# Kernel optimization log

Hardware: AMD Instinct MI355X
Metric: run time of the kernel (lower is better)

The kernel has to match this reference:

```python
import jax, jax.numpy as jnp
import numpy as np

N_HEAD = 16
ROPE_BASE = 10000.0


def rotate_half(x):
    d = x.shape[-1] // 2
    return jnp.concatenate((-x[..., d:], x[..., :d]), axis=-1)


def rope_cos_sin(T, head_dim, dtype):
    inv_freq = 1.0 / (ROPE_BASE ** (jnp.arange(0, head_dim, 2, dtype=jnp.float32) / head_dim))
    t = jnp.arange(T, dtype=jnp.float32)
    freqs = jnp.einsum('i,j->ij', t, inv_freq)  # [T, head_dim/2]
    emb = jnp.concatenate((freqs, freqs), axis=-1)  # [T, head_dim]
    return jnp.cos(emb).astype(dtype), jnp.sin(emb).astype(dtype)


def setup_inputs() -> dict:
    key = jax.random.key(0)
    k1, k2, k3 = jax.random.split(key, 3)
    B, T, C = 4, 2048, 2048
    x = jax.random.normal(k1, (B, T, C), dtype=jnp.float32)
    w_attn = jax.random.normal(k2, (3 * C, C), dtype=jnp.float32) * (1.0 / np.sqrt(C))
    w_proj = jax.random.normal(k3, (C, C), dtype=jnp.float32) * (1.0 / np.sqrt(C))
    return {"x": x, "w_attn": w_attn, "w_proj": w_proj}


def reference(x, w_attn, w_proj):
    B, T, C = x.shape
    H = N_HEAD
    D = C // H
    qkv = jnp.einsum('btc,fc->btf', x, w_attn)  # [B, T, 3C]
    q, k, v = jnp.split(qkv, 3, axis=-1)
    # [B, H, T, D]
    q = q.reshape(B, T, H, D).transpose(0, 2, 1, 3)
    k = k.reshape(B, T, H, D).transpose(0, 2, 1, 3)
    v = v.reshape(B, T, H, D).transpose(0, 2, 1, 3)
    cos, sin = rope_cos_sin(T, D, x.dtype)  # [T, D]
    cos = cos[None, None, :, :]
    sin = sin[None, None, :, :]
    q = q * cos + rotate_half(q) * sin
    k = k * cos + rotate_half(k) * sin
    # bidirectional SDPA
    scale = 1.0 / jnp.sqrt(jnp.asarray(D, dtype=x.dtype))
    att = jnp.einsum('bhtd,bhsd->bhts', q, k) * scale
    att = jax.nn.softmax(att, axis=-1)
    y = jnp.einsum('bhts,bhsd->bhtd', att, v)
    y = y.transpose(0, 2, 1, 3).reshape(B, T, C)
    return jnp.einsum('btc,oc->bto', y, w_proj)
```

## Files before the change

kernel.cpp:

```cpp
#include <hip/hip_runtime.h>

#define DEVINL __device__ __forceinline__

typedef unsigned short u16;
typedef __attribute__((ext_vector_type(8))) __bf16 bf16x8;
typedef __attribute__((ext_vector_type(4))) float f32x4;
typedef __attribute__((ext_vector_type(16))) float f32x16;

struct alignas(8) u16x4 { u16 x, y, z, w; };

#define MFMA16(a, b, c) __builtin_amdgcn_mfma_f32_16x16x32_bf16(a, b, c, 0, 0, 0)
#define MFMA32(a, b, c) __builtin_amdgcn_mfma_f32_32x32x16_bf16(a, b, c, 0, 0, 0)

DEVINL u16 f2bf(float f) {
  unsigned u = __builtin_bit_cast(unsigned, f);
  u += 0x7fffu + ((u >> 16) & 1u);
  return (u16)(u >> 16);
}

DEVINL unsigned cvtpk_bf16(float lo, float hi) {
  unsigned r;
  asm("v_cvt_pk_bf16_f32 %0, %1, %2" : "=v"(r) : "v"(lo), "v"(hi));
  return r;
}

DEVINL void plane_swap(unsigned& a, unsigned& b) {
  asm("v_permlane32_swap_b32 %0, %1" : "+v"(a), "+v"(b));
}

DEVINL void gload_lds16(const u16* g, u16* l) {
  __builtin_amdgcn_global_load_lds((const __attribute__((address_space(1))) void*)g,
                                   (__attribute__((address_space(3))) void*)l,
                                   16, 0, 0);
}

DEVINL bf16x8 frag64(const u16* lds, int row, int cg) {
  int c = cg ^ (row & 7);
  return *(const bf16x8*)(lds + row * 64 + c * 8);
}
DEVINL bf16x8 frag128(const u16* lds, int row, int cg) {
  int c = cg ^ (row & 7);
  return *(const bf16x8*)(lds + row * 128 + c * 8);
}

DEVINL void stage_k512(const u16* g, u16* lds, int wave, int lane) {
#pragma unroll
  for (int t = 0; t < 2; ++t) {
    int r = t * 32 + wave * 4 + (lane >> 4);
    int cg = (lane & 15) ^ (r & 7);
    gload_lds16(g + (size_t)r * 128 + cg * 8, lds + (t * 32 + wave * 4) * 128);
  }
}
DEVINL void stage_v512(const u16* g, int ldg, u16* lds, int wave, int lane) {
#pragma unroll
  for (int t = 0; t < 2; ++t) {
    int r = t * 64 + wave * 8 + (lane >> 3);
    int cg = (lane & 7) ^ (r & 7);
    gload_lds16(g + (size_t)r * ldg + cg * 8, lds + (t * 64 + wave * 8) * 64);
  }
}

DEVINL int perm32(int row) { return (row & 3) ^ ((row >> 2) & 3); }

DEVINL void stage32(const u16* g, int ldg, u16* lds, int q, int wave, int lane) {
  int row = q * 128 + wave * 16 + (lane >> 2);
  int cg = (lane & 3) ^ perm32(row);
  gload_lds16(g + (size_t)row * ldg + cg * 8, lds + (q * 128 + wave * 16) * 32);
}

DEVINL bf16x8 frag32(const u16* lds, int row, int lc) {
  int c = lc ^ perm32(row);
  return *(const bf16x8*)(lds + row * 32 + c * 8);
}

__global__ void __launch_bounds__(256) k_cast(const float* __restrict__ src,
                                              u16* __restrict__ dst, int n4) {
  int i = blockIdx.x * blockDim.x + threadIdx.x;
  int stride = gridDim.x * blockDim.x;
  for (; i < n4; i += stride) {
    float4 f = ((const float4*)src)[i];
    u16x4 u;
    u.x = f2bf(f.x); u.y = f2bf(f.y); u.z = f2bf(f.z); u.w = f2bf(f.w);
    ((u16x4*)dst)[i] = u;
  }
}

DEVINL void gemm_loop256(const u16* Ag, const u16* Bg, int K, u16* smem,
                         f32x4 acc[8][4], int wave, int lane) {
  const int wm = wave >> 2, wn = wave & 3;
  const int lr = lane & 15, lc = lane >> 4;

#pragma unroll
  for (int t = 0; t < 3; ++t) {
    u16* At = smem + t * 8192;
    u16* Bt = smem + 32768 + t * 8192;
    stage32(Ag + t * 32, K, At, 0, wave, lane);
    stage32(Ag + t * 32, K, At, 1, wave, lane);
    stage32(Bg + t * 32, K, Bt, 0, wave, lane);
    stage32(Bg + t * 32, K, Bt, 1, wave, lane);
  }
  asm volatile("s_waitcnt vmcnt(8)" ::: "memory");
  asm volatile("s_barrier" ::: "memory");

  bf16x8 bfr[4], aA[4], aB[4];
#pragma unroll
  for (int nf = 0; nf < 4; ++nf)
    bfr[nf] = frag32(smem + 32768, nf * 64 + wn * 16 + lr, lc);
#pragma unroll
  for (int mf = 0; mf < 4; ++mf)
    aA[mf] = frag32(smem, wm * 128 + mf * 16 + lr, lc);

  const int nsteps = K / 32;
  for (int s = 0; s < nsteps; ++s) {
    const int slot = s & 3;
    const u16* Ac = smem + slot * 8192;
    const bool do_stage = (s + 3 < nsteps);
    u16* An = smem + ((s + 3) & 3) * 8192;
    u16* Bn = smem + 32768 + ((s + 3) & 3) * 8192;
    const u16* Agn = Ag + (size_t)(s + 3) * 32;
    const u16* Bgn = Bg + (size_t)(s + 3) * 32;

    __builtin_amdgcn_s_setprio(1);
#pragma unroll
    for (int mf = 0; mf < 4; ++mf)
#pragma unroll
      for (int nf = 0; nf < 4; ++nf)
        acc[mf][nf] = MFMA16(aA[mf], bfr[nf], acc[mf][nf]);
    __builtin_amdgcn_s_setprio(0);
#pragma unroll
    for (int mf = 0; mf < 4; ++mf)
      aB[mf] = frag32(Ac, wm * 128 + (mf + 4) * 16 + lr, lc);
    if (do_stage) {
      stage32(Agn, K, An, 0, wave, lane);
      stage32(Agn, K, An, 1, wave, lane);
    }
    if (s + 3 < nsteps) {
      asm volatile("s_waitcnt vmcnt(6)" ::: "memory");
    } else if (s + 2 < nsteps) {
      asm volatile("s_waitcnt vmcnt(4)" ::: "memory");
    } else if (s + 1 < nsteps) {
      asm volatile("s_waitcnt vmcnt(0)" ::: "memory");
    }
    asm volatile("s_barrier" ::: "memory");

    __builtin_amdgcn_s_setprio(1);
#pragma unroll
    for (int mf = 0; mf < 4; ++mf)
#pragma unroll
      for (int nf = 0; nf < 4; ++nf)
        acc[mf + 4][nf] = MFMA16(aB[mf], bfr[nf], acc[mf + 4][nf]);
    __builtin_amdgcn_s_setprio(0);
    if (s + 1 < nsteps) {
      const int slot1 = (s + 1) & 3;
      const u16* An1 = smem + slot1 * 8192;
      const u16* Bn1 = smem + 32768 + slot1 * 8192;
#pragma unroll
      for (int nf = 0; nf < 4; ++nf)
        bfr[nf] = frag32(Bn1, nf * 64 + wn * 16 + lr, lc);
#pragma unroll
      for (int mf = 0; mf < 4; ++mf)
        aA[mf] = frag32(An1, wm * 128 + mf * 16 + lr, lc);
    }
    if (do_stage) {
      stage32(Bgn, K, Bn, 0, wave, lane);
      stage32(Bgn, K, Bn, 1, wave, lane);
    }
    asm volatile("s_barrier" ::: "memory");
  }
}

__global__ void __launch_bounds__(512, 2) k_gemm_qkv(const u16* __restrict__ xb,
                                                     const u16* __restrict__ wab,
                                                     u16* __restrict__ qb,
                                                     u16* __restrict__ kb,
                                                     u16* __restrict__ vtb) {
  extern __shared__ u16 smem[];
  int bid = blockIdx.x;
  const int xcd = bid & 7, local = bid >> 3;
  const int tm = (xcd & 3) * 8 + (local & 7);
  const int tn = (xcd >> 2) * 12 + (local >> 3);
  const int wave = threadIdx.x >> 6, lane = threadIdx.x & 63;
  const int wm = wave >> 2, wn = wave & 3;
  const int lr = lane & 15, lc = lane >> 4;

  f32x4 acc[8][4];
#pragma unroll
  for (int i = 0; i < 8; ++i)
#pragma unroll
    for (int n = 0; n < 4; ++n) acc[i][n] = f32x4{0.f, 0.f, 0.f, 0.f};

  gemm_loop256(xb + (size_t)tm * 256 * 2048, wab + (size_t)tn * 256 * 2048, 2048,
               smem, acc, wave, lane);

  const int sel = tn >> 3;
  const int hh = (tn & 7) * 2;
  const int m0 = tm * 256 + wm * 128;
  const int b = (tm * 256) >> 11;

  if (sel < 2) {
    u16* dst = sel ? kb : qb;
    const float qs = sel ? 1.0f : 0.12751745f;
    const int d = wn * 16 + lr;
    const float invf = __expf(-0.14391156631f * (float)d);
#pragma unroll
    for (int mf = 0; mf < 8; ++mf) {
#pragma unroll
      for (int j = 0; j < 4; ++j) {
        int t = (m0 + mf * 16 + lc * 4 + j) & 2047;
        float ang = (float)t * invf;
        float s, c;
        __sincosf(ang, &s, &c);
#pragma unroll
        for (int hp = 0; hp < 2; ++hp) {
          float lo = acc[mf][2 * hp][j];
          float hi = acc[mf][2 * hp + 1][j];
          size_t rowp = ((size_t)(b * 16 + hh + hp) * 2048 + t) * 128;
          dst[rowp + d] = f2bf((lo * c - hi * s) * qs);
          dst[rowp + d + 64] = f2bf((hi * c + lo * s) * qs);
        }
      }
    }
  } else {
#pragma unroll
    for (int mf = 0; mf < 8; ++mf) {
      int t0 = (m0 + mf * 16 + lc * 4) & 2047;
#pragma unroll
      for (int nf = 0; nf < 4; ++nf) {
        int d = wn * 16 + lr + (nf & 1) * 64;
        int h = hh + (nf >> 1);
        u16x4 pk;
        pk.x = f2bf(acc[mf][nf][0]);
        pk.y = f2bf(acc[mf][nf][1]);
        pk.z = f2bf(acc[mf][nf][2]);
        pk.w = f2bf(acc[mf][nf][3]);
        *(u16x4*)(vtb + ((size_t)(b * 16 + h) * 128 + d) * 2048 + t0) = pk;
      }
    }
  }
}

__global__ void __launch_bounds__(512, 2) k_gemm_proj(const u16* __restrict__ yb,
                                                      const u16* __restrict__ wpb,
                                                      float* __restrict__ out) {
  extern __shared__ u16 smem[];
  int bid = blockIdx.x;
  int sw = (bid & 7) * 32 + (bid >> 3);
  const int tm = sw >> 3, tn = sw & 7;
  const int wave = threadIdx.x >> 6, lane = threadIdx.x & 63;
  const int wm = wave >> 2, wn = wave & 3;
  const int lr = lane & 15, lc = lane >> 4;

  f32x4 acc[8][4];
#pragma unroll
  for (int i = 0; i < 8; ++i)
#pragma unroll
    for (int n = 0; n < 4; ++n) acc[i][n] = f32x4{0.f, 0.f, 0.f, 0.f};

  gemm_loop256(yb + (size_t)tm * 256 * 2048, wpb + (size_t)tn * 256 * 2048, 2048,
               smem, acc, wave, lane);

  const int m0 = tm * 256 + wm * 128;
#pragma unroll
  for (int mf = 0; mf < 8; ++mf) {
#pragma unroll
    for (int j = 0; j < 4; ++j) {
      int gr = m0 + mf * 16 + lc * 4 + j;
      float* op = out + (size_t)gr * 2048 + tn * 256 + wn * 16 + lr;
#pragma unroll
      for (int nf = 0; nf < 4; ++nf) op[nf * 64] = acc[mf][nf][j];
    }
  }
}

__global__ void __launch_bounds__(512) k_attn(const u16* __restrict__ qg,
                                              const u16* __restrict__ kg,
                                              const u16* __restrict__ vtg,
                                              u16* __restrict__ yg) {
  __shared__ u16 Ks[2][64 * 128];
  __shared__ u16 Vs[2][128 * 64];
  int bid = blockIdx.x;
  int sw = (bid & 7) * 64 + (bid >> 3);
  const int qt = sw & 7, bh = sw >> 3;
  const int wave = threadIdx.x >> 6, lane = threadIdx.x & 63;
  const int hi = lane >> 5, ln = lane & 31;

  const u16* qbh = qg + (size_t)bh * (2048 * 128);
  const u16* kbh = kg + (size_t)bh * (2048 * 128);
  const u16* vbh = vtg + (size_t)bh * (128 * 2048);
  const int qrow0 = qt * 256 + wave * 32;

  bf16x8 qf[8];
#pragma unroll
  for (int kc = 0; kc < 8; ++kc)
    qf[kc] = *(const bf16x8*)(qbh + (size_t)(qrow0 + ln) * 128 + kc * 16 + hi * 8);

  f32x16 yacc[4];
#pragma unroll
  for (int nd = 0; nd < 4; ++nd)
#pragma unroll
    for (int r = 0; r < 16; ++r) yacc[nd][r] = 0.f;
  float m = -1e30f, l = 0.f;

  stage_k512(kbh, Ks[0], wave, lane);
  stage_v512(vbh, 2048, Vs[0], wave, lane);
  __syncthreads();

  int buf = 0;
  for (int kv0 = 0; kv0 < 2048; kv0 += 64) {
    if (kv0 + 64 < 2048) {
      stage_k512(kbh + (size_t)(kv0 + 64) * 128, Ks[buf ^ 1], wave, lane);
      stage_v512(vbh + kv0 + 64, 2048, Vs[buf ^ 1], wave, lane);
    }
    const u16* Kb = Ks[buf];
    const u16* Vb = Vs[buf];

    f32x16 st[2];
#pragma unroll
    for (int h2 = 0; h2 < 2; ++h2)
#pragma unroll
      for (int r = 0; r < 16; ++r) st[h2][r] = 0.f;
    __builtin_amdgcn_s_setprio(1);
#pragma unroll
    for (int kc = 0; kc < 8; ++kc) {
      bf16x8 a0 = frag128(Kb, ln, kc * 2 + hi);
      bf16x8 a1 = frag128(Kb, 32 + ln, kc * 2 + hi);
      st[0] = MFMA32(a0, qf[kc], st[0]);
      st[1] = MFMA32(a1, qf[kc], st[1]);
    }
    __builtin_amdgcn_s_setprio(0);

    float t8[8];
#pragma unroll
    for (int i = 0; i < 8; ++i)
      t8[i] = fmaxf(fmaxf(st[0][i], st[0][i + 8]), fmaxf(st[1][i], st[1][i + 8]));
    float pmax = fmaxf(fmaxf(fmaxf(t8[0], t8[4]), fmaxf(t8[1], t8[5])),
                       fmaxf(fmaxf(t8[2], t8[6]), fmaxf(t8[3], t8[7])));
    pmax = fmaxf(pmax, __shfl_xor(pmax, 32));

    if (__any(pmax - m > 11.5415603f)) {
      float mn = fmaxf(m, pmax);
      float al = __builtin_amdgcn_exp2f(m - mn);
      m = mn;
      l *= al;
#pragma unroll
      for (int nd = 0; nd < 4; ++nd)
#pragma unroll
        for (int r = 0; r < 16; ++r) yacc[nd][r] *= al;
    }

    float sa0 = 0.f, sa1 = 0.f, sa2 = 0.f, sa3 = 0.f;
#pragma unroll
    for (int h2 = 0; h2 < 2; ++h2) {
#pragma unroll
      for (int r = 0; r < 16; ++r) {
        float e = __builtin_amdgcn_exp2f(st[h2][r] - m);
        st[h2][r] = e;
        if ((r & 3) == 0) sa0 += e;
        else if ((r & 3) == 1) sa1 += e;
        else if ((r & 3) == 2) sa2 += e;
        else sa3 += e;
      }
    }
    float ssum = (sa0 + sa1) + (sa2 + sa3);
    ssum += __shfl_xor(ssum, 32);
    l += ssum;

    unsigned wa[2][4], wb[2][4];
#pragma unroll
    for (int h2 = 0; h2 < 2; ++h2)
#pragma unroll
      for (int q8 = 0; q8 < 4; ++q8) {
        wa[h2][q8] = cvtpk_bf16(st[h2][q8 * 4 + 0], st[h2][q8 * 4 + 1]);
        wb[h2][q8] = cvtpk_bf16(st[h2][q8 * 4 + 2], st[h2][q8 * 4 + 3]);
      }

    __builtin_amdgcn_s_setprio(1);
#pragma unroll
    for (int ks = 0; ks < 4; ++ks) {
      const int h2 = ks >> 1, k1 = ks & 1;
      unsigned w0 = wa[h2][2 * k1], w2 = wa[h2][2 * k1 + 1];
      plane_swap(w0, w2);
      unsigned w1 = wb[h2][2 * k1], w3 = wb[h2][2 * k1 + 1];
      plane_swap(w1, w3);
      union { unsigned u[4]; bf16x8 v; } pa;
      pa.u[0] = w0; pa.u[1] = w1; pa.u[2] = w2; pa.u[3] = w3;
#pragma unroll
      for (int nd = 0; nd < 4; ++nd) {
        bf16x8 bv = frag64(Vb, nd * 32 + ln, 2 * ks + hi);
        yacc[nd] = MFMA32(pa.v, bv, yacc[nd]);
      }
    }
    __builtin_amdgcn_s_setprio(0);

    __syncthreads();
    buf ^= 1;
  }

  const int b = bh >> 4, h = bh & 15;
  float inv = 1.f / l;
#pragma unroll
  for (int r = 0; r < 16; ++r) {
    int crow = (r & 3) + 8 * (r >> 2) + 4 * hi;
    float li = __shfl(inv, crow);
    int t = qrow0 + crow;
    size_t rp = ((size_t)b * 2048 + t) * 2048 + h * 128;
#pragma unroll
    for (int nd = 0; nd < 4; ++nd)
      yg[rp + nd * 32 + ln] = f2bf(yacc[nd][r] * li);
  }
}

extern "C" void kernel_launch(void* const* d_in, const int* in_sizes, int n_in,
                              void* d_out, int out_size, void* d_ws, size_t ws_size,
                              hipStream_t stream) {
  const float* x = (const float*)d_in[0];
  const float* wa = (const float*)d_in[1];
  const float* wp = (const float*)d_in[2];
  float* out = (float*)d_out;

  u16* xb = (u16*)d_ws;
  u16* wab = xb + 16777216;
  u16* wpb = wab + 12582912;
  u16* qb = wpb + 4194304;
  u16* kb = qb + 16777216;
  u16* vtb = kb + 16777216;
  u16* yb = vtb + 16777216;

  hipFuncSetAttribute((const void*)k_gemm_qkv,
                      hipFuncAttributeMaxDynamicSharedMemorySize, 131072);
  hipFuncSetAttribute((const void*)k_gemm_proj,
                      hipFuncAttributeMaxDynamicSharedMemorySize, 131072);

  k_cast<<<dim3(2048), dim3(256), 0, stream>>>(x, xb, 4194304);
  k_cast<<<dim3(2048), dim3(256), 0, stream>>>(wa, wab, 3145728);
  k_cast<<<dim3(1024), dim3(256), 0, stream>>>(wp, wpb, 1048576);
  k_gemm_qkv<<<dim3(768), dim3(512), 131072, stream>>>(xb, wab, qb, kb, vtb);
  k_attn<<<dim3(512), dim3(512), 0, stream>>>(qb, kb, vtb, yb);
  k_gemm_proj<<<dim3(256), dim3(512), 131072, stream>>>(yb, wpb, out);
}
```

Measured before the change: 454.7 us.

## Switch GEMM mainloop to double-buffered LDS and merge cast kernels

Replaces the 4-slot, 3-deep prefetch pipeline in the shared GEMM loop with a 2-slot double buffer, cutting dynamic LDS per block from 128KB to 64KB. With launch_bounds(512,2) this makes it possible to fit more blocks per CU. The three fp32-to-bf16 cast launches are merged into one kernel that splits its blocks by range. In exchange, prefetch depth drops to one step and each iteration now does a full vmcnt(0) wait, so global-load latency is less hidden.

```diff
diff --git a/kernel.cpp b/kernel.cpp
--- a/kernel.cpp
+++ b/kernel.cpp
@@ -73,15 +73,31 @@
   return *(const bf16x8*)(lds + row * 32 + c * 8);
 }
 
-__global__ void __launch_bounds__(256) k_cast(const float* __restrict__ src,
-                                              u16* __restrict__ dst, int n4) {
-  int i = blockIdx.x * blockDim.x + threadIdx.x;
-  int stride = gridDim.x * blockDim.x;
-  for (; i < n4; i += stride) {
-    float4 f = ((const float4*)src)[i];
+__global__ void __launch_bounds__(256) k_cast3(const float4* __restrict__ x,
+                                               const float4* __restrict__ wa,
+                                               const float4* __restrict__ wp,
+                                               u16x4* __restrict__ xb,
+                                               u16x4* __restrict__ wab,
+                                               u16x4* __restrict__ wpb) {
+  const int b = blockIdx.x;
+  const float4* src;
+  u16x4* dst;
+  int n, i, stride;
+  if (b < 1024) {
+    src = x; dst = xb; n = 4194304;
+    i = b * 256 + threadIdx.x; stride = 1024 * 256;
+  } else if (b < 1792) {
+    src = wa; dst = wab; n = 3145728;
+    i = (b - 1024) * 256 + threadIdx.x; stride = 768 * 256;
+  } else {
+    src = wp; dst = wpb; n = 1048576;
+    i = (b - 1792) * 256 + threadIdx.x; stride = 256 * 256;
+  }
+  for (; i < n; i += stride) {
+    float4 f = src[i];
     u16x4 u;
     u.x = f2bf(f.x); u.y = f2bf(f.y); u.z = f2bf(f.z); u.w = f2bf(f.w);
-    ((u16x4*)dst)[i] = u;
+    dst[i] = u;
   }
 }
 
@@ -89,37 +105,36 @@
                          f32x4 acc[8][4], int wave, int lane) {
   const int wm = wave >> 2, wn = wave & 3;
   const int lr = lane & 15, lc = lane >> 4;
-
-#pragma unroll
-  for (int t = 0; t < 3; ++t) {
-    u16* At = smem + t * 8192;
-    u16* Bt = smem + 32768 + t * 8192;
-    stage32(Ag + t * 32, K, At, 0, wave, lane);
-    stage32(Ag + t * 32, K, At, 1, wave, lane);
-    stage32(Bg + t * 32, K, Bt, 0, wave, lane);
-    stage32(Bg + t * 32, K, Bt, 1, wave, lane);
-  }
-  asm volatile("s_waitcnt vmcnt(8)" ::: "memory");
+  u16* Bs = smem + 16384;
+
+  stage32(Ag, K, smem, 0, wave, lane);
+  stage32(Ag, K, smem, 1, wave, lane);
+  stage32(Bg, K, Bs, 0, wave, lane);
+  stage32(Bg, K, Bs, 1, wave, lane);
+  asm volatile("s_waitcnt vmcnt(0)" ::: "memory");
   asm volatile("s_barrier" ::: "memory");
 
   bf16x8 bfr[4], aA[4], aB[4];
 #pragma unroll
   for (int nf = 0; nf < 4; ++nf)
-    bfr[nf] = frag32(smem + 32768, nf * 64 + wn * 16 + lr, lc);
+    bfr[nf] = frag32(Bs, nf * 64 + wn * 16 + lr, lc);
 #pragma unroll
   for (int mf = 0; mf < 4; ++mf)
     aA[mf] = frag32(smem, wm * 128 + mf * 16 + lr, lc);
 
   const int nsteps = K / 32;
   for (int s = 0; s < nsteps; ++s) {
-    const int slot = s & 3;
-    const u16* Ac = smem + slot * 8192;
-    const bool do_stage = (s + 3 < nsteps);
-    u16* An = smem + ((s + 3) & 3) * 8192;
-    u16* Bn = smem + 32768 + ((s + 3) & 3) * 8192;
-    const u16* Agn = Ag + (size_t)(s + 3) * 32;
-    const u16* Bgn = Bg + (size_t)(s + 3) * 32;
-
+    const u16* Ac = smem + (s & 1) * 8192;
+    u16* An = smem + ((s + 1) & 1) * 8192;
+    u16* Bn = Bs + ((s + 1) & 1) * 8192;
+    const bool more = (s + 1 < nsteps);
+    const u16* Agn = Ag + (size_t)(s + 1) * 32;
+    const u16* Bgn = Bg + (size_t)(s + 1) * 32;
+
+    if (more) {
+      stage32(Agn, K, An, 0, wave, lane);
+      stage32(Agn, K, An, 1, wave, lane);
+    }
     __builtin_amdgcn_s_setprio(1);
 #pragma unroll
     for (int mf = 0; mf < 4; ++mf)
@@ -130,19 +145,11 @@
 #pragma unroll
     for (int mf = 0; mf < 4; ++mf)
       aB[mf] = frag32(Ac, wm * 128 + (mf + 4) * 16 + lr, lc);
-    if (do_stage) {
-      stage32(Agn, K, An, 0, wave, lane);
-      stage32(Agn, K, An, 1, wave, lane);
-    }
-    if (s + 3 < nsteps) {
-      asm volatile("s_waitcnt vmcnt(6)" ::: "memory");
-    } else if (s + 2 < nsteps) {
-      asm volatile("s_waitcnt vmcnt(4)" ::: "memory");
-    } else if (s + 1 < nsteps) {
-      asm volatile("s_waitcnt vmcnt(0)" ::: "memory");
-    }
-    asm volatile("s_barrier" ::: "memory");
-
+
+    if (more) {
+      stage32(Bgn, K, Bn, 0, wave, lane);
+      stage32(Bgn, K, Bn, 1, wave, lane);
+    }
     __builtin_amdgcn_s_setprio(1);
 #pragma unroll
     for (int mf = 0; mf < 4; ++mf)
@@ -150,22 +157,16 @@
       for (int nf = 0; nf < 4; ++nf)
         acc[mf + 4][nf] = MFMA16(aB[mf], bfr[nf], acc[mf + 4][nf]);
     __builtin_amdgcn_s_setprio(0);
-    if (s + 1 < nsteps) {
-      const int slot1 = (s + 1) & 3;
-      const u16* An1 = smem + slot1 * 8192;
-      const u16* Bn1 = smem + 32768 + slot1 * 8192;
+    if (more) {
+      asm volatile("s_waitcnt vmcnt(0)" ::: "memory");
+      asm volatile("s_barrier" ::: "memory");
 #pragma unroll
       for (int nf = 0; nf < 4; ++nf)
-        bfr[nf] = frag32(Bn1, nf * 64 + wn * 16 + lr, lc);
+        bfr[nf] = frag32(Bn, nf * 64 + wn * 16 + lr, lc);
 #pragma unroll
       for (int mf = 0; mf < 4; ++mf)
-        aA[mf] = frag32(An1, wm * 128 + mf * 16 + lr, lc);
-    }
-    if (do_stage) {
-      stage32(Bgn, K, Bn, 0, wave, lane);
-      stage32(Bgn, K, Bn, 1, wave, lane);
-    }
-    asm volatile("s_barrier" ::: "memory");
+        aA[mf] = frag32(An, wm * 128 + mf * 16 + lr, lc);
+    }
   }
 }
 
@@ -427,14 +428,14 @@
   u16* yb = vtb + 16777216;
 
   hipFuncSetAttribute((const void*)k_gemm_qkv,
-                      hipFuncAttributeMaxDynamicSharedMemorySize, 131072);
+                      hipFuncAttributeMaxDynamicSharedMemorySize, 65536);
   hipFuncSetAttribute((const void*)k_gemm_proj,
-                      hipFuncAttributeMaxDynamicSharedMemorySize, 131072);
-
-  k_cast<<<dim3(2048), dim3(256), 0, stream>>>(x, xb, 4194304);
-  k_cast<<<dim3(2048), dim3(256), 0, stream>>>(wa, wab, 3145728);
-  k_cast<<<dim3(1024), dim3(256), 0, stream>>>(wp, wpb, 1048576);
-  k_gemm_qkv<<<dim3(768), dim3(512), 131072, stream>>>(xb, wab, qb, kb, vtb);
+                      hipFuncAttributeMaxDynamicSharedMemorySize, 65536);
+
+  k_cast3<<<dim3(2048), dim3(256), 0, stream>>>(
+      (const float4*)x, (const float4*)wa, (const float4*)wp,
+      (u16x4*)xb, (u16x4*)wab, (u16x4*)wpb);
+  k_gemm_qkv<<<dim3(768), dim3(512), 65536, stream>>>(xb, wab, qb, kb, vtb);
   k_attn<<<dim3(512), dim3(512), 0, stream>>>(qb, kb, vtb, yb);
-  k_gemm_proj<<<dim3(256), dim3(512), 131072, stream>>>(yb, wpb, out);
-}
+  k_gemm_proj<<<dim3(256), dim3(512), 65536, stream>>>(yb, wpb, out);
+}
```

Measured after the change: 456.2 us. No clear change (+0.3%).
